# Optimization experiments

Hardware: AMD Instinct MI355X
Metric: run time of the kernel (lower is better)

Reference implementation:

```python
import jax, jax.numpy as jnp
import numpy as np

EPS = 1e-08

def setup_inputs() -> dict:
    key = jax.random.key(0)
    k1, k2, k3, k4 = jax.random.split(key, 4)
    batch, n_in, n_out, D = 32768, 256, 512, 16
    x = jax.random.uniform(k1, (batch, n_in), jnp.float32, minval=-1.0, maxval=1.0)
    omega = jax.random.normal(k2, (D, 1), jnp.float32)          # stddev=1.0 init
    phase = 0.1 * jax.random.normal(k3, (D, 1), jnp.float32)    # zeros in module; small noise for non-degenerate test
    std_c = 1.0 / np.sqrt(n_in * D)
    c_basis = std_c * jax.random.normal(k4, (n_out, n_in, D), jnp.float32)
    bias = jnp.zeros((n_out,), jnp.float32)
    return {"x": x, "omega": omega, "phase": phase, "c_basis": c_basis, "bias": bias}

def _basis(x, omega, phase):
    # x: (batch, n_in) -> B: (batch, n_in, D)
    D = omega.shape[0]
    w = omega.reshape(1, 1, D)
    p = phase.reshape(1, 1, D)
    wx = w * x[..., None]
    s = jnp.sin(wx + p)
    mu = jnp.exp(-0.5 * w ** 2) * jnp.sin(p)
    std = jnp.sqrt(0.5 * (1.0 - jnp.exp(-2.0 * w ** 2) * jnp.cos(2.0 * p)) - mu ** 2)
    return (s + mu) / (std + EPS)

def reference(x, omega, phase, c_basis, bias):
    B = _basis(x, omega, phase)                     # (batch, n_in, D)
    y = jnp.einsum('bid,oid->bo', B, c_basis)       # (batch, n_out)
    return y + bias
```

## Files before the change

### kernel.cpp

```cpp
#include <hip/hip_runtime.h>
#include <hip/hip_bf16.h>


#define BATCH 32768
#define NIN   256
#define NOUT  512
#define DDIM  16
#define BM    128
#define BN    512
#define BK    64
#define NKT   ((NIN*DDIM)/BK)
#define TILE_BYTES (BN*BK*2)
#define ABYTES (BM*BK*2)
#define BBYTES (BN*BK*2)
#define EPSV  1e-8f
#define INV2PI 0.15915494309189535f

typedef short  bf16x8 __attribute__((ext_vector_type(8)));
typedef float  f32x4  __attribute__((ext_vector_type(4)));

static __device__ __forceinline__ ushort f2bf(float f) {
  union { __hip_bfloat16 h; ushort u; } cv;
  cv.h = __float2bfloat16(f);
  return cv.u;
}

static __device__ __forceinline__ float sgpr_f(float v) {
  return __builtin_bit_cast(float,
      __builtin_amdgcn_readfirstlane(__builtin_bit_cast(int, v)));
}

__global__ __launch_bounds__(256) void prep_kernel(
    const float* __restrict__ omega, const float* __restrict__ phase,
    const float* __restrict__ c_basis, const float* __restrict__ bias,
    ushort* __restrict__ cb, float* __restrict__ offs)
{
  __shared__ float s_scale[DDIM];
  __shared__ float s_musc[DDIM];
  __shared__ float s_red[4];

  const int o = blockIdx.x;
  const int t = threadIdx.x;

  if (t < DDIM) {
    float w = omega[t];
    float p = phase[t];
    float mu  = expf(-0.5f * w * w) * sinf(p);
    float var = 0.5f * (1.0f - expf(-2.0f * w * w) * cosf(2.0f * p)) - mu * mu;
    float sd  = sqrtf(fmaxf(var, 0.0f));
    float sc  = 1.0f / (sd + EPSV);
    s_scale[t] = sc;
    s_musc[t]  = mu * sc;
  }
  __syncthreads();

  const float* cp = c_basis + ((size_t)o * NIN + t) * DDIM;
  float cv[DDIM];
  {
    const float4* cp4 = (const float4*)cp;
    float4 a = cp4[0], b = cp4[1], c = cp4[2], d = cp4[3];
    cv[0]=a.x; cv[1]=a.y; cv[2]=a.z; cv[3]=a.w;
    cv[4]=b.x; cv[5]=b.y; cv[6]=b.z; cv[7]=b.w;
    cv[8]=c.x; cv[9]=c.y; cv[10]=c.z; cv[11]=c.w;
    cv[12]=d.x; cv[13]=d.y; cv[14]=d.z; cv[15]=d.w;
  }

  float partial = 0.0f;
  uint pk[8];
#pragma unroll
  for (int d = 0; d < DDIM; d += 2) {
    partial += cv[d] * s_musc[d] + cv[d+1] * s_musc[d+1];
    ushort u0 = f2bf(cv[d]   * s_scale[d]);
    ushort u1 = f2bf(cv[d+1] * s_scale[d+1]);
    pk[d >> 1] = (uint)u0 | ((uint)u1 << 16);
  }

  {
    const int r   = o;
    const int kt  = t >> 2;
    const int swz = (r & 7) << 4;
    char* tile = (char*)cb + (size_t)kt * TILE_BYTES;
    int b0 = r * 128 + (t & 3) * 32;
    *(uint4*)(tile + ((b0     ) ^ swz)) = make_uint4(pk[0], pk[1], pk[2], pk[3]);
    *(uint4*)(tile + ((b0 + 16) ^ swz)) = make_uint4(pk[4], pk[5], pk[6], pk[7]);
  }

#pragma unroll
  for (int off = 32; off > 0; off >>= 1) partial += __shfl_down(partial, off, 64);
  if ((t & 63) == 0) s_red[t >> 6] = partial;
  __syncthreads();
  if (t == 0) offs[o] = bias[o] + s_red[0] + s_red[1] + s_red[2] + s_red[3];
}

__global__ __launch_bounds__(512, 2) void gemm_kernel(
    const float* __restrict__ x, const float* __restrict__ omega,
    const float* __restrict__ phase, const ushort* __restrict__ cb,
    const float* __restrict__ offs, float* __restrict__ out)
{
  extern __shared__ char lds[];

  const int t    = threadIdx.x;
  const int lane = t & 63;
  const int wid  = t >> 6;
  const int wm   = wid >> 2;
  const int wn   = wid & 3;
  const int row0 = blockIdx.x * BM;

  float wv[DDIM], pv[DDIM];
#pragma unroll
  for (int d = 0; d < DDIM; ++d) {
    wv[d] = sgpr_f(omega[d] * INV2PI);
    pv[d] = sgpr_f(phase[d] * INV2PI);
  }

  f32x4 acc[4][8];
#pragma unroll
  for (int m = 0; m < 4; ++m)
#pragma unroll
    for (int n = 0; n < 8; ++n) acc[m][n] = (f32x4){0.f, 0.f, 0.f, 0.f};

  const int arow = t >> 2;
  const int acol = t & 3;
  const float* xbase = x + (size_t)(row0 + arow) * NIN + acol;
  const int aswz = (arow & 7) << 4;
  const int ab0  = arow * 128 + acol * 32;

  const int hi  = lane >> 4;
  const int l15 = lane & 15;

#define GLL(s_, d_) __builtin_amdgcn_global_load_lds(                          \
      (const __attribute__((address_space(1))) void*)(s_),                     \
      (__attribute__((address_space(3))) void*)(d_), 16, 0, 0)

#define ISSUE_B(kt_, sb_)                                                      \
  {                                                                            \
    const char* src = (const char*)cb + (size_t)(kt_) * TILE_BYTES             \
                      + wid * 8192 + lane * 16;                                \
    char* dst = lds + 32768 + (sb_) * BBYTES + wid * 8192;                     \
    GLL(src, dst);                 GLL(src + 1024, dst + 1024);                \
    GLL(src + 2048, dst + 2048);   GLL(src + 3072, dst + 3072);                \
    GLL(src + 4096, dst + 4096);   GLL(src + 5120, dst + 5120);                \
    GLL(src + 6144, dst + 6144);   GLL(src + 7168, dst + 7168);                \
  }

#define SINS_ALL(xx_)                                                          \
    _Pragma("unroll")                                                          \
    for (int d = 0; d < DDIM; d += 2) {                                        \
      float s0 = __builtin_amdgcn_sinf(fmaf(wv[d],   (xx_), pv[d]));           \
      float s1 = __builtin_amdgcn_sinf(fmaf(wv[d+1], (xx_), pv[d+1]));         \
      uint u0 = __builtin_bit_cast(uint, s0) + 0x8000u;                        \
      uint u1 = __builtin_bit_cast(uint, s1) + 0x8000u;                        \
      pk[d >> 1] = __builtin_amdgcn_perm(u1, u0, 0x07060302u);                 \
    }

#define A_WRITE2(sb_)                                                          \
    *(uint4*)(lds + (sb_) * ABYTES + ((ab0     ) ^ aswz)) =                    \
        make_uint4(pk[0], pk[1], pk[2], pk[3]);                                \
    *(uint4*)(lds + (sb_) * ABYTES + ((ab0 + 16) ^ aswz)) =                    \
        make_uint4(pk[4], pk[5], pk[6], pk[7]);

#define MFMA_STEP(mb_)                                                         \
  {                                                                            \
    const char* AsB = lds + (mb_) * ABYTES;                                    \
    const char* BsB = lds + 32768 + (mb_) * BBYTES;                            \
    __builtin_amdgcn_s_setprio(1);                                             \
    _Pragma("unroll")                                                          \
    for (int kk = 0; kk < 2; ++kk) {                                           \
      bf16x8 af[4];                                                            \
      _Pragma("unroll")                                                        \
      for (int m = 0; m < 4; ++m) {                                            \
        int rr = wm * 64 + m * 16 + l15;                                       \
        af[m] = *(const bf16x8*)(AsB + ((rr*128 + kk*64 + hi*16) ^ ((rr&7)<<4))); \
      }                                                                        \
      _Pragma("unroll")                                                        \
      for (int nh = 0; nh < 2; ++nh) {                                         \
        bf16x8 bfr[4];                                                         \
        _Pragma("unroll")                                                      \
        for (int n4 = 0; n4 < 4; ++n4) {                                       \
          int rr = wn * 128 + (nh * 4 + n4) * 16 + l15;                        \
          bfr[n4] = *(const bf16x8*)(BsB + ((rr*128 + kk*64 + hi*16) ^ ((rr&7)<<4))); \
        }                                                                      \
        _Pragma("unroll")                                                      \
        for (int m = 0; m < 4; ++m)                                            \
          _Pragma("unroll")                                                    \
          for (int n4 = 0; n4 < 4; ++n4)                                       \
            acc[m][nh * 4 + n4] = __builtin_amdgcn_mfma_f32_16x16x32_bf16(     \
                af[m], bfr[n4], acc[m][nh * 4 + n4], 0, 0, 0);                 \
      }                                                                        \
    }                                                                          \
    __builtin_amdgcn_s_setprio(0);                                             \
  }

#define CBAR(vm_)                                                              \
  __builtin_amdgcn_sched_barrier(0);                                           \
  asm volatile("s_waitcnt vmcnt(" #vm_ ") lgkmcnt(0)" ::: "memory");           \
  __builtin_amdgcn_s_barrier();                                                \
  __builtin_amdgcn_sched_barrier(0);

#define BODY(kt_, mb_, sb_, XU_, XL_)                                          \
  {                                                                            \
    ISSUE_B(((kt_) + 1 < NKT ? (kt_) + 1 : NKT - 1), sb_);                     \
    __builtin_amdgcn_sched_barrier(0);                                         \
    XL_ = xbase[((kt_) + 2 < NKT ? (kt_) + 2 : NKT - 1) * 4];                  \
    __builtin_amdgcn_sched_barrier(0);                                         \
    uint pk[8];                                                                \
    SINS_ALL(XU_)                                                              \
    MFMA_STEP(mb_)                                                             \
    A_WRITE2(sb_)                                                              \
    CBAR(1)                                                                    \
  }

  float xs0, xs1;
  {
    float xp = xbase[0];
    __builtin_amdgcn_sched_barrier(0);
    ISSUE_B(0, 0);
    __builtin_amdgcn_sched_barrier(0);
    xs1 = xbase[4];
    __builtin_amdgcn_sched_barrier(0);
    {
      uint pk[8];
      SINS_ALL(xp)
      A_WRITE2(0)
    }
    CBAR(1)
  }

  for (int kt = 0; kt < NKT; kt += 2) {
    BODY(kt,     0, 1, xs1, xs0)
    BODY(kt + 1, 1, 0, xs0, xs1)
  }

#pragma unroll
  for (int n = 0; n < 8; ++n) {
    int col = wn * 128 + n * 16 + l15;
    float off = offs[col];
#pragma unroll
    for (int m = 0; m < 4; ++m) {
      int row = row0 + wm * 64 + m * 16 + hi * 4;
      float* op = out + (size_t)row * NOUT + col;
#pragma unroll
      for (int j = 0; j < 4; ++j)
        op[(size_t)j * NOUT] = acc[m][n][j] + off;
    }
  }
}

extern "C" void kernel_launch(void* const* d_in, const int* in_sizes, int n_in,
                              void* d_out, int out_size, void* d_ws, size_t ws_size,
                              hipStream_t stream) {
  const float* x       = (const float*)d_in[0];
  const float* omega   = (const float*)d_in[1];
  const float* phase   = (const float*)d_in[2];
  const float* c_basis = (const float*)d_in[3];
  const float* bias    = (const float*)d_in[4];
  float* out = (float*)d_out;

  float*  offs = (float*)d_ws;
  ushort* cb   = (ushort*)((char*)d_ws + 2048);

  hipFuncSetAttribute((const void*)gemm_kernel,
                      hipFuncAttributeMaxDynamicSharedMemorySize, 163840);

  prep_kernel<<<NOUT, 256, 0, stream>>>(omega, phase, c_basis, bias, cb, offs);
  gemm_kernel<<<BATCH / BM, 512, 163840, stream>>>(x, omega, phase, cb, offs, out);
}
```

Before: 131.9 us.

## Load B fragments directly from global into registers in MFMA layout

Measured after the change: 493.3 us. +274.0%, slower.

```diff
diff --git a/kernel.cpp b/kernel.cpp
--- a/kernel.cpp
+++ b/kernel.cpp
@@ -10,9 +10,7 @@
 #define BN    512
 #define BK    64
 #define NKT   ((NIN*DDIM)/BK)
-#define TILE_BYTES (BN*BK*2)
 #define ABYTES (BM*BK*2)
-#define BBYTES (BN*BK*2)
 #define EPSV  1e-8f
 #define INV2PI 0.15915494309189535f
 
@@ -76,13 +74,15 @@
   }
 
   {
-    const int r   = o;
     const int kt  = t >> 2;
-    const int swz = (r & 7) << 4;
-    char* tile = (char*)cb + (size_t)kt * TILE_BYTES;
-    int b0 = r * 128 + (t & 3) * 32;
-    *(uint4*)(tile + ((b0     ) ^ swz)) = make_uint4(pk[0], pk[1], pk[2], pk[3]);
-    *(uint4*)(tile + ((b0 + 16) ^ swz)) = make_uint4(pk[4], pk[5], pk[6], pk[7]);
+    const int sec = t & 3;
+    const int kk  = sec >> 1;
+    const int hi0 = (sec & 1) * 2;
+    const int nt  = o >> 4;
+    const int l15 = o & 15;
+    char* base = (char*)cb + (size_t)kt * 65536 + nt * 2048 + kk * 1024;
+    *(uint4*)(base + (hi0 * 16 + l15) * 16)       = make_uint4(pk[0], pk[1], pk[2], pk[3]);
+    *(uint4*)(base + ((hi0 + 1) * 16 + l15) * 16) = make_uint4(pk[4], pk[5], pk[6], pk[7]);
   }
 
 #pragma unroll
@@ -128,20 +128,13 @@
   const int hi  = lane >> 4;
   const int l15 = lane & 15;
 
-#define GLL(s_, d_) __builtin_amdgcn_global_load_lds(                          \
-      (const __attribute__((address_space(1))) void*)(s_),                     \
-      (__attribute__((address_space(3))) void*)(d_), 16, 0, 0)
-
-#define ISSUE_B(kt_, sb_)                                                      \
-  {                                                                            \
-    const char* src = (const char*)cb + (size_t)(kt_) * TILE_BYTES             \
-                      + wid * 8192 + lane * 16;                                \
-    char* dst = lds + 32768 + (sb_) * BBYTES + wid * 8192;                     \
-    GLL(src, dst);                 GLL(src + 1024, dst + 1024);                \
-    GLL(src + 2048, dst + 2048);   GLL(src + 3072, dst + 3072);                \
-    GLL(src + 4096, dst + 4096);   GLL(src + 5120, dst + 5120);                \
-    GLL(src + 6144, dst + 6144);   GLL(src + 7168, dst + 7168);                \
-  }
+  const char* cbW = (const char*)cb + (wn * 8) * 2048 + lane * 16;
+
+#define BLOAD(dst_, kt_, kk_)                                                  \
+    _Pragma("unroll")                                                          \
+    for (int n = 0; n < 8; ++n)                                                \
+      dst_[n] = *(const bf16x8*)(cbW + (size_t)(kt_) * 65536                   \
+                                  + n * 2048 + (kk_) * 1024);
 
 #define SINS_ALL(xx_)                                                          \
     _Pragma("unroll")                                                          \
@@ -159,71 +152,54 @@
     *(uint4*)(lds + (sb_) * ABYTES + ((ab0 + 16) ^ aswz)) =                    \
         make_uint4(pk[4], pk[5], pk[6], pk[7]);
 
-#define MFMA_STEP(mb_)                                                         \
+#define MFMA_HALF(mb_, kk_, bfr_)                                              \
   {                                                                            \
     const char* AsB = lds + (mb_) * ABYTES;                                    \
-    const char* BsB = lds + 32768 + (mb_) * BBYTES;                            \
+    bf16x8 af[4];                                                              \
+    _Pragma("unroll")                                                          \
+    for (int m = 0; m < 4; ++m) {                                              \
+      int rr = wm * 64 + m * 16 + l15;                                         \
+      af[m] = *(const bf16x8*)(AsB + ((rr*128 + (kk_)*64 + hi*16) ^ ((rr&7)<<4))); \
+    }                                                                          \
     __builtin_amdgcn_s_setprio(1);                                             \
     _Pragma("unroll")                                                          \
-    for (int kk = 0; kk < 2; ++kk) {                                           \
-      bf16x8 af[4];                                                            \
+    for (int m = 0; m < 4; ++m)                                                \
       _Pragma("unroll")                                                        \
-      for (int m = 0; m < 4; ++m) {                                            \
-        int rr = wm * 64 + m * 16 + l15;                                       \
-        af[m] = *(const bf16x8*)(AsB + ((rr*128 + kk*64 + hi*16) ^ ((rr&7)<<4))); \
-      }                                                                        \
-      _Pragma("unroll")                                                        \
-      for (int nh = 0; nh < 2; ++nh) {                                         \
-        bf16x8 bfr[4];                                                         \
-        _Pragma("unroll")                                                      \
-        for (int n4 = 0; n4 < 4; ++n4) {                                       \
-          int rr = wn * 128 + (nh * 4 + n4) * 16 + l15;                        \
-          bfr[n4] = *(const bf16x8*)(BsB + ((rr*128 + kk*64 + hi*16) ^ ((rr&7)<<4))); \
-        }                                                                      \
-        _Pragma("unroll")                                                      \
-        for (int m = 0; m < 4; ++m)                                            \
-          _Pragma("unroll")                                                    \
-          for (int n4 = 0; n4 < 4; ++n4)                                       \
-            acc[m][nh * 4 + n4] = __builtin_amdgcn_mfma_f32_16x16x32_bf16(     \
-                af[m], bfr[n4], acc[m][nh * 4 + n4], 0, 0, 0);                 \
-      }                                                                        \
-    }                                                                          \
+      for (int n = 0; n < 8; ++n)                                              \
+        acc[m][n] = __builtin_amdgcn_mfma_f32_16x16x32_bf16(af[m], bfr_[n], acc[m][n], 0, 0, 0); \
     __builtin_amdgcn_s_setprio(0);                                             \
   }
-
-#define CBAR(vm_)                                                              \
-  __builtin_amdgcn_sched_barrier(0);                                           \
-  asm volatile("s_waitcnt vmcnt(" #vm_ ") lgkmcnt(0)" ::: "memory");           \
-  __builtin_amdgcn_s_barrier();                                                \
-  __builtin_amdgcn_sched_barrier(0);
 
 #define BODY(kt_, mb_, sb_, XU_, XL_)                                          \
   {                                                                            \
-    ISSUE_B(((kt_) + 1 < NKT ? (kt_) + 1 : NKT - 1), sb_);                     \
-    __builtin_amdgcn_sched_barrier(0);                                         \
+    BLOAD(bfrB, kt_, 1)                                                        \
     XL_ = xbase[((kt_) + 2 < NKT ? (kt_) + 2 : NKT - 1) * 4];                  \
-    __builtin_amdgcn_sched_barrier(0);                                         \
+    MFMA_HALF(mb_, 0, bfrA)                                                    \
     uint pk[8];                                                                \
     SINS_ALL(XU_)                                                              \
-    MFMA_STEP(mb_)                                                             \
+    BLOAD(bfrA, ((kt_) + 1 < NKT ? (kt_) + 1 : NKT - 1), 0)                    \
+    MFMA_HALF(mb_, 1, bfrB)                                                    \
     A_WRITE2(sb_)                                                              \
-    CBAR(1)                                                                    \
-  }
+    __builtin_amdgcn_sched_barrier(0);                                         \
+    asm volatile("s_waitcnt lgkmcnt(0)" ::: "memory");                         \
+    __builtin_amdgcn_s_barrier();                                              \
+    __builtin_amdgcn_sched_barrier(0);                                         \
+  }
+
+  bf16x8 bfrA[8], bfrB[8];
 
   float xs0, xs1;
   {
     float xp = xbase[0];
+    BLOAD(bfrA, 0, 0)
+    xs1 = xbase[4];
+    uint pk[8];
+    SINS_ALL(xp)
+    A_WRITE2(0)
     __builtin_amdgcn_sched_barrier(0);
-    ISSUE_B(0, 0);
+    asm volatile("s_waitcnt lgkmcnt(0)" ::: "memory");
+    __builtin_amdgcn_s_barrier();
     __builtin_amdgcn_sched_barrier(0);
-    xs1 = xbase[4];
-    __builtin_amdgcn_sched_barrier(0);
-    {
-      uint pk[8];
-      SINS_ALL(xp)
-      A_WRITE2(0)
-    }
-    CBAR(1)
   }
 
   for (int kt = 0; kt < NKT; kt += 2) {
@@ -259,9 +235,6 @@
   float*  offs = (float*)d_ws;
   ushort* cb   = (ushort*)((char*)d_ws + 2048);
 
-  hipFuncSetAttribute((const void*)gemm_kernel,
-                      hipFuncAttributeMaxDynamicSharedMemorySize, 163840);
-
   prep_kernel<<<NOUT, 256, 0, stream>>>(omega, phase, c_basis, bias, cb, offs);
-  gemm_kernel<<<BATCH / BM, 512, 163840, stream>>>(x, omega, phase, cb, offs, out);
-}
+  gemm_kernel<<<BATCH / BM, 512, 32768, stream>>>(x, omega, phase, cb, offs, out);
+}
```

## Shrink GEMM tiles to 64x256 and split N across blocks

Applied to the files above, without the earlier changes.

Measured after the change: 159.5 us. 1.21x slower.

```diff
diff --git a/kernel.cpp b/kernel.cpp
--- a/kernel.cpp
+++ b/kernel.cpp
@@ -6,8 +6,8 @@
 #define NIN   256
 #define NOUT  512
 #define DDIM  16
-#define BM    128
-#define BN    512
+#define BM    64
+#define BN    256
 #define BK    64
 #define NKT   ((NIN*DDIM)/BK)
 #define TILE_BYTES (BN*BK*2)
@@ -76,10 +76,11 @@
   }
 
   {
-    const int r   = o;
-    const int kt  = t >> 2;
-    const int swz = (r & 7) << 4;
-    char* tile = (char*)cb + (size_t)kt * TILE_BYTES;
+    const int r     = o & (BN - 1);
+    const int n_blk = o >> 8;
+    const int kt    = t >> 2;
+    const int swz   = (r & 7) << 4;
+    char* tile = (char*)cb + (size_t)(n_blk * NKT + kt) * TILE_BYTES;
     int b0 = r * 128 + (t & 3) * 32;
     *(uint4*)(tile + ((b0     ) ^ swz)) = make_uint4(pk[0], pk[1], pk[2], pk[3]);
     *(uint4*)(tile + ((b0 + 16) ^ swz)) = make_uint4(pk[4], pk[5], pk[6], pk[7]);
@@ -92,7 +93,7 @@
   if (t == 0) offs[o] = bias[o] + s_red[0] + s_red[1] + s_red[2] + s_red[3];
 }
 
-__global__ __launch_bounds__(512, 2) void gemm_kernel(
+__global__ __launch_bounds__(256, 2) void gemm_kernel(
     const float* __restrict__ x, const float* __restrict__ omega,
     const float* __restrict__ phase, const ushort* __restrict__ cb,
     const float* __restrict__ offs, float* __restrict__ out)
@@ -101,10 +102,11 @@
 
   const int t    = threadIdx.x;
   const int lane = t & 63;
-  const int wid  = t >> 6;
-  const int wm   = wid >> 2;
-  const int wn   = wid & 3;
-  const int row0 = blockIdx.x * BM;
+  const int wn   = t >> 6;
+  const int bm   = blockIdx.x >> 1;
+  const int bn   = blockIdx.x & 1;
+  const int row0 = bm * BM;
+  const int col0 = bn * BN;
 
   float wv[DDIM], pv[DDIM];
 #pragma unroll
@@ -113,11 +115,11 @@
     pv[d] = sgpr_f(phase[d] * INV2PI);
   }
 
-  f32x4 acc[4][8];
+  f32x4 acc[4][4];
 #pragma unroll
   for (int m = 0; m < 4; ++m)
 #pragma unroll
-    for (int n = 0; n < 8; ++n) acc[m][n] = (f32x4){0.f, 0.f, 0.f, 0.f};
+    for (int n = 0; n < 4; ++n) acc[m][n] = (f32x4){0.f, 0.f, 0.f, 0.f};
 
   const int arow = t >> 2;
   const int acol = t & 3;
@@ -128,15 +130,16 @@
   const int hi  = lane >> 4;
   const int l15 = lane & 15;
 
+  const char* cbB = (const char*)cb + (size_t)bn * NKT * TILE_BYTES;
+
 #define GLL(s_, d_) __builtin_amdgcn_global_load_lds(                          \
       (const __attribute__((address_space(1))) void*)(s_),                     \
       (__attribute__((address_space(3))) void*)(d_), 16, 0, 0)
 
 #define ISSUE_B(kt_, sb_)                                                      \
   {                                                                            \
-    const char* src = (const char*)cb + (size_t)(kt_) * TILE_BYTES             \
-                      + wid * 8192 + lane * 16;                                \
-    char* dst = lds + 32768 + (sb_) * BBYTES + wid * 8192;                     \
+    const char* src = cbB + (size_t)(kt_) * TILE_BYTES + wn * 8192 + lane*16;  \
+    char* dst = lds + 16384 + (sb_) * BBYTES + wn * 8192;                      \
     GLL(src, dst);                 GLL(src + 1024, dst + 1024);                \
     GLL(src + 2048, dst + 2048);   GLL(src + 3072, dst + 3072);                \
     GLL(src + 4096, dst + 4096);   GLL(src + 5120, dst + 5120);                \
@@ -162,31 +165,26 @@
 #define MFMA_STEP(mb_)                                                         \
   {                                                                            \
     const char* AsB = lds + (mb_) * ABYTES;                                    \
-    const char* BsB = lds + 32768 + (mb_) * BBYTES;                            \
+    const char* BsB = lds + 16384 + (mb_) * BBYTES;                            \
     __builtin_amdgcn_s_setprio(1);                                             \
     _Pragma("unroll")                                                          \
     for (int kk = 0; kk < 2; ++kk) {                                           \
-      bf16x8 af[4];                                                            \
+      bf16x8 af[4], bfr[4];                                                    \
       _Pragma("unroll")                                                        \
       for (int m = 0; m < 4; ++m) {                                            \
-        int rr = wm * 64 + m * 16 + l15;                                       \
+        int rr = m * 16 + l15;                                                 \
         af[m] = *(const bf16x8*)(AsB + ((rr*128 + kk*64 + hi*16) ^ ((rr&7)<<4))); \
       }                                                                        \
       _Pragma("unroll")                                                        \
-      for (int nh = 0; nh < 2; ++nh) {                                         \
-        bf16x8 bfr[4];                                                         \
+      for (int n = 0; n < 4; ++n) {                                            \
+        int rr = wn * 64 + n * 16 + l15;                                       \
+        bfr[n] = *(const bf16x8*)(BsB + ((rr*128 + kk*64 + hi*16) ^ ((rr&7)<<4))); \
+      }                                                                        \
+      _Pragma("unroll")                                                        \
+      for (int m = 0; m < 4; ++m)                                              \
         _Pragma("unroll")                                                      \
-        for (int n4 = 0; n4 < 4; ++n4) {                                       \
-          int rr = wn * 128 + (nh * 4 + n4) * 16 + l15;                        \
-          bfr[n4] = *(const bf16x8*)(BsB + ((rr*128 + kk*64 + hi*16) ^ ((rr&7)<<4))); \
-        }                                                                      \
-        _Pragma("unroll")                                                      \
-        for (int m = 0; m < 4; ++m)                                            \
-          _Pragma("unroll")                                                    \
-          for (int n4 = 0; n4 < 4; ++n4)                                       \
-            acc[m][nh * 4 + n4] = __builtin_amdgcn_mfma_f32_16x16x32_bf16(     \
-                af[m], bfr[n4], acc[m][nh * 4 + n4], 0, 0, 0);                 \
-      }                                                                        \
+        for (int n = 0; n < 4; ++n)                                            \
+          acc[m][n] = __builtin_amdgcn_mfma_f32_16x16x32_bf16(af[m], bfr[n], acc[m][n], 0, 0, 0); \
     }                                                                          \
     __builtin_amdgcn_s_setprio(0);                                             \
   }
@@ -232,12 +230,12 @@
   }
 
 #pragma unroll
-  for (int n = 0; n < 8; ++n) {
-    int col = wn * 128 + n * 16 + l15;
+  for (int n = 0; n < 4; ++n) {
+    int col = col0 + wn * 64 + n * 16 + l15;
     float off = offs[col];
 #pragma unroll
     for (int m = 0; m < 4; ++m) {
-      int row = row0 + wm * 64 + m * 16 + hi * 4;
+      int row = row0 + m * 16 + hi * 4;
       float* op = out + (size_t)row * NOUT + col;
 #pragma unroll
       for (int j = 0; j < 4; ++j)
@@ -260,8 +258,8 @@
   ushort* cb   = (ushort*)((char*)d_ws + 2048);
 
   hipFuncSetAttribute((const void*)gemm_kernel,
-                      hipFuncAttributeMaxDynamicSharedMemorySize, 163840);
+                      hipFuncAttributeMaxDynamicSharedMemorySize, 81920);
 
   prep_kernel<<<NOUT, 256, 0, stream>>>(omega, phase, c_basis, bias, cb, offs);
-  gemm_kernel<<<BATCH / BM, 512, 163840, stream>>>(x, omega, phase, cb, offs, out);
-}
+  gemm_kernel<<<(BATCH / BM) * (NOUT / BN), 256, 81920, stream>>>(x, omega, phase, cb, offs, out);
+}
```
